# Kernel optimization log

Measured on AMD Instinct MI355X. Metric: run time of the kernel, lower is better.

The kernel has to match this reference:

```python
import jax, jax.numpy as jnp
import numpy as np

NOISE_EPS = 0.01
LB_COEFF = 0.01
TOP_K = 2


def setup_inputs() -> dict:
    key = jax.random.key(0)
    k1, k2, k3 = jax.random.split(key, 3)
    B, S, H, E = 4, 4096, 4096, 8
    x = jax.random.normal(k1, (B, S, H), dtype=jnp.float32)
    W = jax.random.normal(k2, (H, E), dtype=jnp.float32) * (1.0 / np.sqrt(H))
    b = jnp.zeros((E,), dtype=jnp.float32)
    noise = jax.random.normal(k3, (B * S, E), dtype=jnp.float32)
    return {"x": x, "W": W, "b": b, "noise": noise}


def reference(x, W, b, noise):
    B, S, H = x.shape
    E = W.shape[1]
    x_flat = x.reshape(-1, H)                      # [BS, H]
    logits = x_flat @ W + b + noise * NOISE_EPS    # [BS, E]
    routing_weights = jax.nn.softmax(logits, axis=-1)
    top_k_weights, top_k_indices = jax.lax.top_k(routing_weights, TOP_K)
    top_k_weights = top_k_weights / jnp.sum(top_k_weights, axis=-1, keepdims=True)
    # load-balancing aux loss
    expert_usage = jnp.mean(routing_weights, axis=0)        # [E]
    target = 1.0 / E
    aux_loss = LB_COEFF * jnp.sum((expert_usage - target) ** 2)
    return (top_k_weights.reshape(B, S, TOP_K),
            top_k_indices.reshape(B, S, TOP_K),
            aux_loss)
```

## Files before the change

kernel.cpp:

```cpp
#include <hip/hip_runtime.h>


#define BS      16384
#define HDIM    4096
#define NE      8
#define RPW     4
#define NWAVE   16
#define NITER   (HDIM / 4 / 64)
#define NOISE_EPS 0.01f
#define LB_COEFF  0.01f

__global__ __launch_bounds__(1024, 4)
void router_main(const float* __restrict__ x, const float* __restrict__ W,
                 const float* __restrict__ bias, const float* __restrict__ noise,
                 float* __restrict__ out, float* __restrict__ usage_ws) {
    const int tid  = threadIdx.x;
    const int lane = tid & 63;
    const int wave = tid >> 6;
    const int row0 = blockIdx.x * (NWAVE * RPW) + wave * RPW;

    __shared__ float4 w_lds[HDIM * 2];
    __shared__ float block_usage[NE];
    if (tid < NE) block_usage[tid] = 0.0f;
    {
        const float4* __restrict__ W4 = (const float4*)W;
#pragma unroll
        for (int i = tid; i < HDIM * 2; i += 1024) {
            const int f = i >> 3, j = i & 7;
            w_lds[(i & ~7) | (j ^ (f & 7))] = W4[i];
        }
    }
    __syncthreads();

    float acc[RPW][NE];
#pragma unroll
    for (int r = 0; r < RPW; ++r)
#pragma unroll
        for (int e = 0; e < NE; ++e) acc[r][e] = 0.0f;

    const float4* __restrict__ x4 = (const float4*)(x + (size_t)row0 * HDIM);
    const int wxor = lane & 7;

    float4 xa[RPW], xb[RPW];
#pragma unroll
    for (int r = 0; r < RPW; ++r)
        xa[r] = x4[(size_t)r * (HDIM / 4) + lane];

#define FMA_HALF(XC, F, KK)                                                   \
    {                                                                         \
        float4 wr[4];                                                         \
        _Pragma("unroll")                                                     \
        for (int m = 0; m < 4; ++m)                                           \
            wr[m] = w_lds[(F) * 8 + ((4 * (KK) + m) ^ wxor)];                 \
        _Pragma("unroll")                                                     \
        for (int r = 0; r < RPW; ++r) {                                       \
            _Pragma("unroll")                                                 \
            for (int kq = 0; kq < 2; ++kq) {                                  \
                const int k = 2 * (KK) + kq;                                  \
                const float xv = ((const float*)&XC[r])[k];                   \
                acc[r][0] += xv * wr[2 * kq].x;                               \
                acc[r][1] += xv * wr[2 * kq].y;                               \
                acc[r][2] += xv * wr[2 * kq].z;                               \
                acc[r][3] += xv * wr[2 * kq].w;                               \
                acc[r][4] += xv * wr[2 * kq + 1].x;                           \
                acc[r][5] += xv * wr[2 * kq + 1].y;                           \
                acc[r][6] += xv * wr[2 * kq + 1].z;                           \
                acc[r][7] += xv * wr[2 * kq + 1].w;                           \
            }                                                                 \
        }                                                                     \
    }

#pragma unroll 1
    for (int it = 0; it < NITER; it += 2) {
        {
            const int fn = (it + 1) * 64 + lane;
#pragma unroll
            for (int r = 0; r < RPW; ++r)
                xb[r] = x4[(size_t)r * (HDIM / 4) + fn];
            const int f = it * 64 + lane;
            FMA_HALF(xa, f, 0)
            FMA_HALF(xa, f, 1)
        }
        {
            const int fn = ((it + 2 < NITER) ? (it + 2) : (NITER - 1)) * 64 + lane;
#pragma unroll
            for (int r = 0; r < RPW; ++r)
                xa[r] = x4[(size_t)r * (HDIM / 4) + fn];
            const int f = (it + 1) * 64 + lane;
            FMA_HALF(xb, f, 0)
            FMA_HALF(xb, f, 1)
        }
    }
#undef FMA_HALF

#pragma unroll
    for (int r = 0; r < RPW; ++r)
#pragma unroll
        for (int e = 0; e < NE; ++e) {
            float v = acc[r][e];
#pragma unroll
            for (int m = 1; m < 64; m <<= 1) v += __shfl_xor(v, m, 64);
            acc[r][e] = v;
        }

    if (lane < RPW) {
        const int row = row0 + lane;

        float logits[NE];
#pragma unroll
        for (int r = 0; r < RPW; ++r)
            if (lane == r)
#pragma unroll
                for (int e = 0; e < NE; ++e) logits[e] = acc[r][e];

        const float4 b_lo = ((const float4*)bias)[0];
        const float4 b_hi = ((const float4*)bias)[1];
        const float4 n_lo = ((const float4*)(noise + (size_t)row * NE))[0];
        const float4 n_hi = ((const float4*)(noise + (size_t)row * NE))[1];

        logits[0] += b_lo.x + NOISE_EPS * n_lo.x;
        logits[1] += b_lo.y + NOISE_EPS * n_lo.y;
        logits[2] += b_lo.z + NOISE_EPS * n_lo.z;
        logits[3] += b_lo.w + NOISE_EPS * n_lo.w;
        logits[4] += b_hi.x + NOISE_EPS * n_hi.x;
        logits[5] += b_hi.y + NOISE_EPS * n_hi.y;
        logits[6] += b_hi.z + NOISE_EPS * n_hi.z;
        logits[7] += b_hi.w + NOISE_EPS * n_hi.w;

        float m = logits[0];
#pragma unroll
        for (int e = 1; e < NE; ++e) m = fmaxf(m, logits[e]);
        float p[NE], s = 0.0f;
#pragma unroll
        for (int e = 0; e < NE; ++e) { p[e] = expf(logits[e] - m); s += p[e]; }
        const float inv_s = 1.0f / s;

        float v1 = p[0]; int e1 = 0;
#pragma unroll
        for (int e = 1; e < NE; ++e) if (p[e] > v1) { v1 = p[e]; e1 = e; }
        float v2 = -1.0f; int e2 = 0;
#pragma unroll
        for (int e = 0; e < NE; ++e)
            if (e != e1 && p[e] > v2) { v2 = p[e]; e2 = e; }

        const float inv_d = 1.0f / (v1 + v2);
        out[(size_t)row * 2]     = v1 * inv_d;
        out[(size_t)row * 2 + 1] = v2 * inv_d;
        out[(size_t)(BS * 2) + row * 2]     = (float)e1;
        out[(size_t)(BS * 2) + row * 2 + 1] = (float)e2;

#pragma unroll
        for (int e = 0; e < NE; ++e)
            atomicAdd(&block_usage[e], p[e] * inv_s);
    }

    __syncthreads();
    if (tid < NE) atomicAdd(usage_ws + tid, block_usage[tid]);
}

__global__ void router_finalize(const float* __restrict__ usage_ws,
                                float* __restrict__ out) {
    if (threadIdx.x == 0) {
        float aux = 0.0f;
#pragma unroll
        for (int e = 0; e < NE; ++e) {
            const float mean = usage_ws[e] * (1.0f / (float)BS);
            const float d = mean - (1.0f / (float)NE);
            aux += d * d;
        }
        out[(size_t)BS * 4] = LB_COEFF * aux;
    }
}

extern "C" void kernel_launch(void* const* d_in, const int* in_sizes, int n_in,
                              void* d_out, int out_size, void* d_ws, size_t ws_size,
                              hipStream_t stream) {
    const float* x     = (const float*)d_in[0];
    const float* W     = (const float*)d_in[1];
    const float* b     = (const float*)d_in[2];
    const float* noise = (const float*)d_in[3];
    float* out = (float*)d_out;
    float* usage = (float*)d_ws;

    hipMemsetAsync(usage, 0, NE * sizeof(float), stream);

    const int blocks = BS / (NWAVE * RPW);
    router_main<<<blocks, 1024, 0, stream>>>(x, W, b, noise, out, usage);
    router_finalize<<<1, 64, 0, stream>>>(usage, out);
}
```

Baseline: 371.5 us.

## Triple-buffer x loads with per-wave staggered chunks and replace atomics with partial sums

The x streaming loop now uses three register buffers, keeping two chunk loads in flight while one is computed. Each wave starts at a different chunk offset, which spreads LDS and memory access across waves. The global atomic usage accumulation and its memset are replaced by per-block partial sums that a one-wave finalize kernel reduces with shuffles. The deeper prefetch costs extra VGPRs, which under the 1024-thread launch bound could cause spills or lower occupancy.

```diff
diff --git a/kernel.cpp b/kernel.cpp
--- a/kernel.cpp
+++ b/kernel.cpp
@@ -6,14 +6,14 @@
 #define NE      8
 #define RPW     4
 #define NWAVE   16
-#define NITER   (HDIM / 4 / 64)
+#define NITER   16
 #define NOISE_EPS 0.01f
 #define LB_COEFF  0.01f
 
 __global__ __launch_bounds__(1024, 4)
 void router_main(const float* __restrict__ x, const float* __restrict__ W,
                  const float* __restrict__ bias, const float* __restrict__ noise,
-                 float* __restrict__ out, float* __restrict__ usage_ws) {
+                 float* __restrict__ out, float* __restrict__ part) {
     const int tid  = threadIdx.x;
     const int lane = tid & 63;
     const int wave = tid >> 6;
@@ -24,7 +24,6 @@
     if (tid < NE) block_usage[tid] = 0.0f;
     {
         const float4* __restrict__ W4 = (const float4*)W;
-#pragma unroll
         for (int i = tid; i < HDIM * 2; i += 1024) {
             const int f = i >> 3, j = i & 7;
             w_lds[(i & ~7) | (j ^ (f & 7))] = W4[i];
@@ -38,13 +37,20 @@
 #pragma unroll
         for (int e = 0; e < NE; ++e) acc[r][e] = 0.0f;
 
-    const float4* __restrict__ x4 = (const float4*)(x + (size_t)row0 * HDIM);
+    const float4* __restrict__ x4 = (const float4*)x + (size_t)row0 * (HDIM / 4);
     const int wxor = lane & 7;
 
-    float4 xa[RPW], xb[RPW];
-#pragma unroll
-    for (int r = 0; r < RPW; ++r)
-        xa[r] = x4[(size_t)r * (HDIM / 4) + lane];
+    float4 bufA[RPW], bufB[RPW], bufC[RPW];
+
+#define CHUNKC(k) (((k) + wave) & 15)
+
+#define LOADTO(BUF, k)                                                        \
+    {                                                                         \
+        const int o_ = CHUNKC(k) * 64 + lane;                                 \
+        _Pragma("unroll")                                                     \
+        for (int r = 0; r < RPW; ++r)                                         \
+            BUF[r] = x4[r * (HDIM / 4) + o_];                                 \
+    }
 
 #define FMA_HALF(XC, F, KK)                                                   \
     {                                                                         \
@@ -70,28 +76,33 @@
         }                                                                     \
     }
 
+#define BODY(BUF, k)                                                          \
+    {                                                                         \
+        const int F_ = CHUNKC(k) * 64 + lane;                                 \
+        FMA_HALF(BUF, F_, 0)                                                  \
+        FMA_HALF(BUF, F_, 1)                                                  \
+    }
+
+    LOADTO(bufA, 0)
+    LOADTO(bufB, 1)
+    LOADTO(bufC, 2)
+
 #pragma unroll 1
-    for (int it = 0; it < NITER; it += 2) {
-        {
-            const int fn = (it + 1) * 64 + lane;
-#pragma unroll
-            for (int r = 0; r < RPW; ++r)
-                xb[r] = x4[(size_t)r * (HDIM / 4) + fn];
-            const int f = it * 64 + lane;
-            FMA_HALF(xa, f, 0)
-            FMA_HALF(xa, f, 1)
-        }
-        {
-            const int fn = ((it + 2 < NITER) ? (it + 2) : (NITER - 1)) * 64 + lane;
-#pragma unroll
-            for (int r = 0; r < RPW; ++r)
-                xa[r] = x4[(size_t)r * (HDIM / 4) + fn];
-            const int f = (it + 1) * 64 + lane;
-            FMA_HALF(xb, f, 0)
-            FMA_HALF(xb, f, 1)
-        }
-    }
+    for (int s = 0; s < 4; ++s) {
+        const int k0 = 3 * s;
+        BODY(bufA, k0)     LOADTO(bufA, k0 + 3)
+        BODY(bufB, k0 + 1) LOADTO(bufB, k0 + 4)
+        BODY(bufC, k0 + 2) LOADTO(bufC, k0 + 5)
+    }
+    BODY(bufA, 12) LOADTO(bufA, 15)
+    BODY(bufB, 13)
+    BODY(bufC, 14)
+    BODY(bufA, 15)
+
+#undef BODY
 #undef FMA_HALF
+#undef LOADTO
+#undef CHUNKC
 
 #pragma unroll
     for (int r = 0; r < RPW; ++r)
@@ -155,16 +166,33 @@
     }
 
     __syncthreads();
-    if (tid < NE) atomicAdd(usage_ws + tid, block_usage[tid]);
+    if (tid < NE) part[blockIdx.x * NE + tid] = block_usage[tid];
 }
 
-__global__ void router_finalize(const float* __restrict__ usage_ws,
+__global__ void router_finalize(const float* __restrict__ part,
                                 float* __restrict__ out) {
-    if (threadIdx.x == 0) {
+    const int lane = threadIdx.x & 63;
+    float p[NE];
+#pragma unroll
+    for (int e = 0; e < NE; ++e) p[e] = 0.0f;
+#pragma unroll
+    for (int j = 0; j < 4; ++j) {
+        const int b = lane * 4 + j;
+#pragma unroll
+        for (int e = 0; e < NE; ++e) p[e] += part[b * NE + e];
+    }
+#pragma unroll
+    for (int e = 0; e < NE; ++e) {
+        float v = p[e];
+#pragma unroll
+        for (int m = 1; m < 64; m <<= 1) v += __shfl_xor(v, m, 64);
+        p[e] = v;
+    }
+    if (lane == 0) {
         float aux = 0.0f;
 #pragma unroll
         for (int e = 0; e < NE; ++e) {
-            const float mean = usage_ws[e] * (1.0f / (float)BS);
+            const float mean = p[e] * (1.0f / (float)BS);
             const float d = mean - (1.0f / (float)NE);
             aux += d * d;
         }
@@ -179,12 +207,10 @@
     const float* W     = (const float*)d_in[1];
     const float* b     = (const float*)d_in[2];
     const float* noise = (const float*)d_in[3];
-    float* out = (float*)d_out;
-    float* usage = (float*)d_ws;
-
-    hipMemsetAsync(usage, 0, NE * sizeof(float), stream);
+    float* out  = (float*)d_out;
+    float* part = (float*)d_ws;
 
     const int blocks = BS / (NWAVE * RPW);
-    router_main<<<blocks, 1024, 0, stream>>>(x, W, b, noise, out, usage);
-    router_finalize<<<1, 64, 0, stream>>>(usage, out);
+    router_main<<<blocks, 1024, 0, stream>>>(x, W, b, noise, out, part);
+    router_finalize<<<1, 64, 0, stream>>>(part, out);
 }
```

New measurement: 392.4 us. 1.06x slower.
